# Kernel optimization log

Hardware: AMD Instinct MI355X
Metric: run time of the kernel (lower is better)

## Reference

```python
import jax, jax.numpy as jnp
import numpy as np

B, N = 4096, 512


def setup_inputs() -> dict:
    key = jax.random.key(0)
    ks = jax.random.split(key, 8)
    waypoints = jax.random.normal(ks[0], (B, N, 2), dtype=jnp.float32)
    # learned params: scalar smooth_weight + curvature_net MLP (4->64->32->1)
    smooth_weight = jnp.float32(0.3)
    W1 = jax.random.normal(ks[1], (4, 64), dtype=jnp.float32) * 0.5
    b1 = jnp.zeros((64,), dtype=jnp.float32)
    W2 = jax.random.normal(ks[2], (64, 32), dtype=jnp.float32) * 0.125
    b2 = jnp.zeros((32,), dtype=jnp.float32)
    W3 = jax.random.normal(ks[3], (32, 1), dtype=jnp.float32) * 0.18
    b3 = jnp.zeros((1,), dtype=jnp.float32)
    return {"waypoints": waypoints, "smooth_weight": smooth_weight,
            "W1": W1, "b1": b1, "W2": W2, "b2": b2, "W3": W3, "b3": b3}


def _forward(waypoints, smooth_weight, W1, b1, W2, b2, W3, b3):
    Bq, Nq, _ = waypoints.shape
    # finite differences
    d1 = waypoints[:, 1:] - waypoints[:, :-1]          # (B, N-1, 2)
    d2 = d1[:, 1:] - d1[:, :-1]                        # (B, N-2, 2)
    d1 = jnp.concatenate([d1, d1[:, -1:]], axis=1)     # (B, N, 2)
    z = jnp.zeros((Bq, 1, 2), dtype=waypoints.dtype)
    d2 = jnp.concatenate([z, d2, z], axis=1)           # (B, N, 2)
    feats = jnp.concatenate([d1, d2], axis=-1)         # (B, N, 4)
    # curvature MLP -> sigmoid weight in (0,1)
    h = jax.nn.relu(jnp.einsum('bnf,fh->bnh', feats, W1) + b1)
    h = jax.nn.relu(jnp.einsum('bnh,hk->bnk', h, W2) + b2)
    cw = jax.nn.sigmoid(jnp.einsum('bnk,ko->bno', h, W3) + b3)  # (B, N, 1)
    sw = jax.nn.sigmoid(smooth_weight)
    w = sw * (1.0 - cw[..., 0])                        # (B, N)
    # linear recurrence: y_i = w_i * y_{i-1} + (1-w_i) * x_i, y_0 = x_0
    a = jnp.swapaxes(w[:, 1:], 0, 1)                   # (N-1, B)
    x = jnp.swapaxes(waypoints[:, 1:], 0, 1)           # (N-1, B, 2)

    def step(carry, inp):
        a_i, x_i = inp
        y = a_i[:, None] * carry + (1.0 - a_i)[:, None] * x_i
        return y, y

    _, ys = jax.lax.scan(step, waypoints[:, 0], (a, x))
    smoothed = jnp.concatenate([waypoints[:, :1], jnp.swapaxes(ys, 0, 1)], axis=1)
    # endpoints pinned to original (start already equals input)
    smoothed = smoothed.at[:, -1].set(waypoints[:, -1])
    return smoothed


def reference(waypoints, smooth_weight, W1, b1, W2, b2, W3, b3):
    return _forward(waypoints, smooth_weight, W1, b1, W2, b2, W3, b3)
```

## Files before the change

kernel.cpp:

```cpp
#include <hip/hip_runtime.h>
#include <math.h>

#define NPT 512
#define BROWS 4096

typedef _Float16 half8  __attribute__((ext_vector_type(8)));
typedef _Float16 h2     __attribute__((ext_vector_type(2)));
typedef float    f32x16 __attribute__((ext_vector_type(16)));

__device__ __forceinline__ float sigmoidf_fast(float x) {
    return 1.0f / (1.0f + __expf(-x));
}

__device__ __forceinline__ h2 pkrtz(float a, float b) {
    return __builtin_bit_cast(h2, __builtin_amdgcn_cvt_pkrtz(a, b));
}

#if __has_builtin(__builtin_amdgcn_fdot2)
__device__ __forceinline__ float fdot2(h2 a, h2 b, float c) {
    return __builtin_amdgcn_fdot2(__builtin_bit_cast(__fp16 __attribute__((ext_vector_type(2))), a),
                                  __builtin_bit_cast(__fp16 __attribute__((ext_vector_type(2))), b),
                                  c, false);
}
#else
__device__ __forceinline__ float fdot2(h2 a, h2 b, float c) {
    c = fmaf((float)a[0], (float)b[0], c);
    c = fmaf((float)a[1], (float)b[1], c);
    return c;
}
#endif

union H8 { half8 v; h2 p[4]; unsigned int w[4]; };

__device__ __forceinline__ f32x16 mfma32(half8 a, half8 b, f32x16 c) {
    return __builtin_amdgcn_mfma_f32_32x32x16_f16(a, b, c, 0, 0, 0);
}

__device__ __forceinline__ void pl32swap(unsigned &a, unsigned &b) {
    asm volatile("v_permlane32_swap_b32 %0, %1" : "+v"(a), "+v"(b));
}

__device__ __forceinline__ half8 makeB2(unsigned p0, unsigned p1,
                                        unsigned p2, unsigned p3) {
    pl32swap(p0, p2);
    pl32swap(p1, p3);
    H8 B; B.w[0] = p0; B.w[1] = p1; B.w[2] = p2; B.w[3] = p3;
    return B.v;
}

__global__ __launch_bounds__(256, 4) void wps_kernel(
    const float* __restrict__ wp,
    const float* __restrict__ sww,
    const float* __restrict__ W1,
    const float* __restrict__ b1,
    const float* __restrict__ W2,
    const float* __restrict__ b2,
    const float* __restrict__ W3,
    const float* __restrict__ b3,
    float* __restrict__ out)
{
    __shared__ float sLg[2][NPT];
    __shared__ float2 sY[2];

    const int t    = threadIdx.x;
    const int lane = t & 63;
    const int wv   = t >> 6;
    const int row0 = blockIdx.x * 2;
    const int c    = lane & 31;
    const int hi   = lane >> 5;

    half8 A1t[2];
    #pragma unroll
    for (int tt = 0; tt < 2; ++tt) {
        H8 a;
        a.w[0] = 0u; a.w[1] = 0u; a.w[2] = 0u; a.w[3] = 0u;
        if (hi == 0) {
            const int ch = tt * 32 + c;
            h2 v0; v0[0] = (_Float16)W1[0 * 64 + ch]; v0[1] = (_Float16)W1[1 * 64 + ch];
            h2 v1; v1[0] = (_Float16)W1[2 * 64 + ch]; v1[1] = (_Float16)W1[3 * 64 + ch];
            h2 v2; v2[0] = (_Float16)b1[ch];          v2[1] = (_Float16)0.f;
            a.p[0] = v0; a.p[1] = v1; a.p[2] = v2;
        }
        A1t[tt] = a.v;
    }
    half8 A2s[4];
    #pragma unroll
    for (int s = 0; s < 4; ++s) {
        H8 a;
        #pragma unroll
        for (int jj = 0; jj < 4; ++jj) {
            const int k = s * 16 + hi * 8 + 2 * jj;
            h2 v; v[0] = (_Float16)W2[k * 32 + c]; v[1] = (_Float16)W2[(k + 1) * 32 + c];
            a.p[jj] = v;
        }
        A2s[s] = a.v;
    }
    h2 b2p[8], w3p[8];
    #pragma unroll
    for (int rr = 0; rr < 8; ++rr) {
        const int q   = 2 * rr;
        const int row = (q & 3) + 8 * (q >> 2) + 4 * hi;
        h2 bv; bv[0] = (_Float16)b2[row]; bv[1] = (_Float16)b2[row + 1];
        h2 wv2; wv2[0] = (_Float16)W3[row]; wv2[1] = (_Float16)W3[row + 1];
        b2p[rr] = bv;
        w3p[rr] = wv2;
    }

    h2 zeroh; zeroh[0] = (_Float16)0.f; zeroh[1] = (_Float16)0.f;
    const f32x16 zero16 = {0.f,0.f,0.f,0.f,0.f,0.f,0.f,0.f,
                           0.f,0.f,0.f,0.f,0.f,0.f,0.f,0.f};

    const int seg = wv * 128;

    #pragma unroll
    for (int r = 0; r < 2; ++r) {
        const float2* P = (const float2*)(wp + (size_t)(row0 + r) * NPT * 2);

        #pragma unroll
        for (int s2 = 0; s2 < 2; ++s2) {
            const int base = seg + s2 * 64;
            const int g    = base + lane;

            float2 p  = P[g];
            float2 pm = P[(g > 0) ? g - 1 : 0];
            float2 pp = P[(g < NPT - 1) ? g + 1 : NPT - 1];
            float d1x, d1y;
            if (g < NPT - 1) { d1x = pp.x - p.x; d1y = pp.y - p.y; }
            else             { d1x = p.x - pm.x; d1y = p.y - pm.y; }
            float d2x = 0.f, d2y = 0.f;
            if (g >= 1 && g <= NPT - 2) {
                d2x = pp.x - 2.f * p.x + pm.x;
                d2y = pp.y - 2.f * p.y + pm.y;
            }
            const int u01 = __builtin_bit_cast(int, pkrtz(d1x, d1y));
            const int u23 = __builtin_bit_cast(int, pkrtz(d2x, d2y));

            #pragma unroll
            for (int T = 0; T < 2; ++T) {
                const unsigned r01 = (unsigned)__shfl(u01, T * 32 + c);
                const unsigned r23 = (unsigned)__shfl(u23, T * 32 + c);
                H8 B1;
                B1.w[0] = r01; B1.w[1] = r23;
                B1.w[2] = 0x00003C00u; B1.w[3] = 0u;

                f32x16 pre0 = mfma32(A1t[0], B1.v, zero16);
                f32x16 pre1 = mfma32(A1t[1], B1.v, zero16);

                unsigned pw0[8], pw1[8];
                #pragma unroll
                for (int rr = 0; rr < 8; ++rr) {
                    pw0[rr] = __builtin_bit_cast(unsigned,
                        __builtin_elementwise_max(pkrtz(pre0[2*rr], pre0[2*rr+1]), zeroh));
                    pw1[rr] = __builtin_bit_cast(unsigned,
                        __builtin_elementwise_max(pkrtz(pre1[2*rr], pre1[2*rr+1]), zeroh));
                }

                f32x16 accA = zero16;
                f32x16 accB = zero16;
                accA = mfma32(A2s[0], makeB2(pw0[0], pw0[1], pw0[2], pw0[3]), accA);
                accB = mfma32(A2s[1], makeB2(pw0[4], pw0[5], pw0[6], pw0[7]), accB);
                accA = mfma32(A2s[2], makeB2(pw1[0], pw1[1], pw1[2], pw1[3]), accA);
                accB = mfma32(A2s[3], makeB2(pw1[4], pw1[5], pw1[6], pw1[7]), accB);

                float v = 0.f;
                #pragma unroll
                for (int rr = 0; rr < 8; ++rr) {
                    h2 tt2 = pkrtz(accA[2*rr] + accB[2*rr],
                                   accA[2*rr+1] + accB[2*rr+1]);
                    tt2 = tt2 + b2p[rr];
                    tt2 = __builtin_elementwise_max(tt2, zeroh);
                    v = fdot2(tt2, w3p[rr], v);
                }
                v += __shfl_xor(v, 32);
                if (lane < 32) sLg[r][base + T * 32 + lane] = v;
            }
        }
    }

    __syncthreads();

    {
        const int rloc = wv >> 1;
        const int half = wv & 1;
        const int row  = row0 + rloc;
        const float2* P = (const float2*)(wp + (size_t)row * NPT * 2);
        const float bias3 = b3[0];
        const float swv   = sigmoidf_fast(sww[0]);

        const int base = half * 256 + lane * 4;
        float wr[4];
        *reinterpret_cast<float4*>(&wr[0]) =
            *reinterpret_cast<const float4*>(&sLg[rloc][base]);

        const float4* P4 = (const float4*)P;
        float2 pts[4];
        #pragma unroll
        for (int s = 0; s < 2; ++s) {
            float4 v = P4[base / 2 + s];
            pts[2 * s].x     = v.x; pts[2 * s].y     = v.y;
            pts[2 * s + 1].x = v.z; pts[2 * s + 1].y = v.w;
        }

        float a4[4], cx4[4], cy4[4];
        float A = 1.f, Cx = 0.f, Cy = 0.f;
        #pragma unroll
        for (int i = 0; i < 4; ++i) {
            const int g = base + i;
            float a = (g == 0) ? 0.f
                               : swv * (1.f - sigmoidf_fast(wr[i] + bias3));
            float cx = (1.f - a) * pts[i].x;
            float cy = (1.f - a) * pts[i].y;
            a4[i] = a; cx4[i] = cx; cy4[i] = cy;
            Cx = fmaf(a, Cx, cx);
            Cy = fmaf(a, Cy, cy);
            A *= a;
        }
        #pragma unroll
        for (int d = 1; d < 64; d <<= 1) {
            float Ap  = __shfl_up(A, d);
            float Cpx = __shfl_up(Cx, d);
            float Cpy = __shfl_up(Cy, d);
            if (lane >= d) {
                Cx = fmaf(A, Cpx, Cx);
                Cy = fmaf(A, Cpy, Cy);
                A *= Ap;
            }
        }
        float Aex  = __shfl_up(A, 1);
        float Cxex = __shfl_up(Cx, 1);
        float Cyex = __shfl_up(Cy, 1);

        float4* orow = (float4*)(out + (size_t)row * NPT * 2);

        if (half == 0) {
            float yx = (lane == 0) ? 0.f : Cxex;
            float yy = (lane == 0) ? 0.f : Cyex;
            float ox[4], oy[4];
            #pragma unroll
            for (int i = 0; i < 4; ++i) {
                yx = fmaf(a4[i], yx, cx4[i]);
                yy = fmaf(a4[i], yy, cy4[i]);
                ox[i] = yx; oy[i] = yy;
            }
            orow[base / 2]     = make_float4(ox[0], oy[0], ox[1], oy[1]);
            orow[base / 2 + 1] = make_float4(ox[2], oy[2], ox[3], oy[3]);
            if (lane == 63) { sY[rloc].x = yx; sY[rloc].y = yy; }
        }

        __syncthreads();

        if (half == 1) {
            const float2 y255 = sY[rloc];
            float yx = (lane == 0) ? y255.x : fmaf(Aex, y255.x, Cxex);
            float yy = (lane == 0) ? y255.y : fmaf(Aex, y255.y, Cyex);
            float ox[4], oy[4];
            #pragma unroll
            for (int i = 0; i < 4; ++i) {
                yx = fmaf(a4[i], yx, cx4[i]);
                yy = fmaf(a4[i], yy, cy4[i]);
                ox[i] = yx; oy[i] = yy;
            }
            if (lane == 63) {
                float2 pe = P[NPT - 1];
                ox[3] = pe.x; oy[3] = pe.y;
            }
            orow[base / 2]     = make_float4(ox[0], oy[0], ox[1], oy[1]);
            orow[base / 2 + 1] = make_float4(ox[2], oy[2], ox[3], oy[3]);
        }
    }
}

extern "C" void kernel_launch(void* const* d_in, const int* in_sizes, int n_in,
                              void* d_out, int out_size, void* d_ws, size_t ws_size,
                              hipStream_t stream) {
    const float* wp  = (const float*)d_in[0];
    const float* sww = (const float*)d_in[1];
    const float* W1  = (const float*)d_in[2];
    const float* b1  = (const float*)d_in[3];
    const float* W2  = (const float*)d_in[4];
    const float* b2  = (const float*)d_in[5];
    const float* W3  = (const float*)d_in[6];
    const float* b3  = (const float*)d_in[7];
    float* out = (float*)d_out;

    wps_kernel<<<BROWS / 2, 256, 0, stream>>>(wp, sww, W1, b1, W2, b2, W3, b3, out);
}
```

Baseline: 27.61 us.

## Process one row per single-wave block and drop cross-wave scan handoff

Changes the work split from 256-thread blocks covering two rows to 64-thread single-wave blocks covering one row. The single wave loops over all eight 64-point segments for the MLP, then scans 8 points per lane with one wave-wide prefix scan. This removes the second block barrier and the shared-memory carry handoff between half-row waves. In exchange, each wave does four times more serial MLP work, so latency hiding relies on having more resident blocks per CU.

Result: slower. 29.31 us (+6.2%).

```diff
diff --git a/kernel.cpp b/kernel.cpp
--- a/kernel.cpp
+++ b/kernel.cpp
@@ -48,7 +48,7 @@
     return B.v;
 }
 
-__global__ __launch_bounds__(256, 4) void wps_kernel(
+__global__ __launch_bounds__(64, 4) void wps_kernel(
     const float* __restrict__ wp,
     const float* __restrict__ sww,
     const float* __restrict__ W1,
@@ -59,13 +59,10 @@
     const float* __restrict__ b3,
     float* __restrict__ out)
 {
-    __shared__ float sLg[2][NPT];
-    __shared__ float2 sY[2];
-
-    const int t    = threadIdx.x;
-    const int lane = t & 63;
-    const int wv   = t >> 6;
-    const int row0 = blockIdx.x * 2;
+    __shared__ float sLg[NPT];
+
+    const int lane = threadIdx.x & 63;
+    const int row  = blockIdx.x;
     const int c    = lane & 31;
     const int hi   = lane >> 5;
 
@@ -98,10 +95,10 @@
     h2 b2p[8], w3p[8];
     #pragma unroll
     for (int rr = 0; rr < 8; ++rr) {
-        const int q   = 2 * rr;
-        const int row = (q & 3) + 8 * (q >> 2) + 4 * hi;
-        h2 bv; bv[0] = (_Float16)b2[row]; bv[1] = (_Float16)b2[row + 1];
-        h2 wv2; wv2[0] = (_Float16)W3[row]; wv2[1] = (_Float16)W3[row + 1];
+        const int q    = 2 * rr;
+        const int drow = (q & 3) + 8 * (q >> 2) + 4 * hi;
+        h2 bv;  bv[0]  = (_Float16)b2[drow]; bv[1]  = (_Float16)b2[drow + 1];
+        h2 wv2; wv2[0] = (_Float16)W3[drow]; wv2[1] = (_Float16)W3[drow + 1];
         b2p[rr] = bv;
         w3p[rr] = wv2;
     }
@@ -110,107 +107,98 @@
     const f32x16 zero16 = {0.f,0.f,0.f,0.f,0.f,0.f,0.f,0.f,
                            0.f,0.f,0.f,0.f,0.f,0.f,0.f,0.f};
 
-    const int seg = wv * 128;
-
-    #pragma unroll
-    for (int r = 0; r < 2; ++r) {
-        const float2* P = (const float2*)(wp + (size_t)(row0 + r) * NPT * 2);
-
-        #pragma unroll
-        for (int s2 = 0; s2 < 2; ++s2) {
-            const int base = seg + s2 * 64;
-            const int g    = base + lane;
-
-            float2 p  = P[g];
-            float2 pm = P[(g > 0) ? g - 1 : 0];
-            float2 pp = P[(g < NPT - 1) ? g + 1 : NPT - 1];
-            float d1x, d1y;
-            if (g < NPT - 1) { d1x = pp.x - p.x; d1y = pp.y - p.y; }
-            else             { d1x = p.x - pm.x; d1y = p.y - pm.y; }
-            float d2x = 0.f, d2y = 0.f;
-            if (g >= 1 && g <= NPT - 2) {
-                d2x = pp.x - 2.f * p.x + pm.x;
-                d2y = pp.y - 2.f * p.y + pm.y;
+    const float2* P = (const float2*)(wp + (size_t)row * NPT * 2);
+
+    #pragma unroll 2
+    for (int s2 = 0; s2 < 8; ++s2) {
+        const int base = s2 * 64;
+        const int g    = base + lane;
+
+        float2 p  = P[g];
+        float2 pm = P[(g > 0) ? g - 1 : 0];
+        float2 pp = P[(g < NPT - 1) ? g + 1 : NPT - 1];
+        float d1x, d1y;
+        if (g < NPT - 1) { d1x = pp.x - p.x; d1y = pp.y - p.y; }
+        else             { d1x = p.x - pm.x; d1y = p.y - pm.y; }
+        float d2x = 0.f, d2y = 0.f;
+        if (g >= 1 && g <= NPT - 2) {
+            d2x = pp.x - 2.f * p.x + pm.x;
+            d2y = pp.y - 2.f * p.y + pm.y;
+        }
+        const int u01 = __builtin_bit_cast(int, pkrtz(d1x, d1y));
+        const int u23 = __builtin_bit_cast(int, pkrtz(d2x, d2y));
+
+        #pragma unroll
+        for (int T = 0; T < 2; ++T) {
+            const unsigned r01 = (unsigned)__shfl(u01, T * 32 + c);
+            const unsigned r23 = (unsigned)__shfl(u23, T * 32 + c);
+            H8 B1;
+            B1.w[0] = r01; B1.w[1] = r23;
+            B1.w[2] = 0x00003C00u; B1.w[3] = 0u;
+
+            f32x16 pre0 = mfma32(A1t[0], B1.v, zero16);
+            f32x16 pre1 = mfma32(A1t[1], B1.v, zero16);
+
+            unsigned pw0[8], pw1[8];
+            #pragma unroll
+            for (int rr = 0; rr < 8; ++rr) {
+                pw0[rr] = __builtin_bit_cast(unsigned,
+                    __builtin_elementwise_max(pkrtz(pre0[2*rr], pre0[2*rr+1]), zeroh));
+                pw1[rr] = __builtin_bit_cast(unsigned,
+                    __builtin_elementwise_max(pkrtz(pre1[2*rr], pre1[2*rr+1]), zeroh));
             }
-            const int u01 = __builtin_bit_cast(int, pkrtz(d1x, d1y));
-            const int u23 = __builtin_bit_cast(int, pkrtz(d2x, d2y));
-
+
+            f32x16 accA = zero16;
+            f32x16 accB = zero16;
+            accA = mfma32(A2s[0], makeB2(pw0[0], pw0[1], pw0[2], pw0[3]), accA);
+            accB = mfma32(A2s[1], makeB2(pw0[4], pw0[5], pw0[6], pw0[7]), accB);
+            accA = mfma32(A2s[2], makeB2(pw1[0], pw1[1], pw1[2], pw1[3]), accA);
+            accB = mfma32(A2s[3], makeB2(pw1[4], pw1[5], pw1[6], pw1[7]), accB);
+
+            float v = 0.f;
             #pragma unroll
-            for (int T = 0; T < 2; ++T) {
-                const unsigned r01 = (unsigned)__shfl(u01, T * 32 + c);
-                const unsigned r23 = (unsigned)__shfl(u23, T * 32 + c);
-                H8 B1;
-                B1.w[0] = r01; B1.w[1] = r23;
-                B1.w[2] = 0x00003C00u; B1.w[3] = 0u;
-
-                f32x16 pre0 = mfma32(A1t[0], B1.v, zero16);
-                f32x16 pre1 = mfma32(A1t[1], B1.v, zero16);
-
-                unsigned pw0[8], pw1[8];
-                #pragma unroll
-                for (int rr = 0; rr < 8; ++rr) {
-                    pw0[rr] = __builtin_bit_cast(unsigned,
-                        __builtin_elementwise_max(pkrtz(pre0[2*rr], pre0[2*rr+1]), zeroh));
-                    pw1[rr] = __builtin_bit_cast(unsigned,
-                        __builtin_elementwise_max(pkrtz(pre1[2*rr], pre1[2*rr+1]), zeroh));
-                }
-
-                f32x16 accA = zero16;
-                f32x16 accB = zero16;
-                accA = mfma32(A2s[0], makeB2(pw0[0], pw0[1], pw0[2], pw0[3]), accA);
-                accB = mfma32(A2s[1], makeB2(pw0[4], pw0[5], pw0[6], pw0[7]), accB);
-                accA = mfma32(A2s[2], makeB2(pw1[0], pw1[1], pw1[2], pw1[3]), accA);
-                accB = mfma32(A2s[3], makeB2(pw1[4], pw1[5], pw1[6], pw1[7]), accB);
-
-                float v = 0.f;
-                #pragma unroll
-                for (int rr = 0; rr < 8; ++rr) {
-                    h2 tt2 = pkrtz(accA[2*rr] + accB[2*rr],
-                                   accA[2*rr+1] + accB[2*rr+1]);
-                    tt2 = tt2 + b2p[rr];
-                    tt2 = __builtin_elementwise_max(tt2, zeroh);
-                    v = fdot2(tt2, w3p[rr], v);
-                }
-                v += __shfl_xor(v, 32);
-                if (lane < 32) sLg[r][base + T * 32 + lane] = v;
+            for (int rr = 0; rr < 8; ++rr) {
+                h2 tt2 = pkrtz(accA[2*rr] + accB[2*rr],
+                               accA[2*rr+1] + accB[2*rr+1]);
+                tt2 = tt2 + b2p[rr];
+                tt2 = __builtin_elementwise_max(tt2, zeroh);
+                v = fdot2(tt2, w3p[rr], v);
             }
+            v += __shfl_xor(v, 32);
+            if (lane < 32) sLg[base + T * 32 + lane] = v;
         }
     }
 
     __syncthreads();
 
     {
-        const int rloc = wv >> 1;
-        const int half = wv & 1;
-        const int row  = row0 + rloc;
-        const float2* P = (const float2*)(wp + (size_t)row * NPT * 2);
         const float bias3 = b3[0];
         const float swv   = sigmoidf_fast(sww[0]);
 
-        const int base = half * 256 + lane * 4;
-        float wr[4];
-        *reinterpret_cast<float4*>(&wr[0]) =
-            *reinterpret_cast<const float4*>(&sLg[rloc][base]);
+        const int base = lane * 8;
+        float wr[8];
+        *reinterpret_cast<float4*>(&wr[0]) = *reinterpret_cast<const float4*>(&sLg[base]);
+        *reinterpret_cast<float4*>(&wr[4]) = *reinterpret_cast<const float4*>(&sLg[base + 4]);
 
         const float4* P4 = (const float4*)P;
-        float2 pts[4];
-        #pragma unroll
-        for (int s = 0; s < 2; ++s) {
-            float4 v = P4[base / 2 + s];
+        float2 pts[8];
+        #pragma unroll
+        for (int s = 0; s < 4; ++s) {
+            float4 v = P4[lane * 4 + s];
             pts[2 * s].x     = v.x; pts[2 * s].y     = v.y;
             pts[2 * s + 1].x = v.z; pts[2 * s + 1].y = v.w;
         }
 
-        float a4[4], cx4[4], cy4[4];
+        float a8[8], cx8[8], cy8[8];
         float A = 1.f, Cx = 0.f, Cy = 0.f;
         #pragma unroll
-        for (int i = 0; i < 4; ++i) {
+        for (int i = 0; i < 8; ++i) {
             const int g = base + i;
             float a = (g == 0) ? 0.f
                                : swv * (1.f - sigmoidf_fast(wr[i] + bias3));
             float cx = (1.f - a) * pts[i].x;
             float cy = (1.f - a) * pts[i].y;
-            a4[i] = a; cx4[i] = cx; cy4[i] = cy;
+            a8[i] = a; cx8[i] = cx; cy8[i] = cy;
             Cx = fmaf(a, Cx, cx);
             Cy = fmaf(a, Cy, cy);
             A *= a;
@@ -226,46 +214,23 @@
                 A *= Ap;
             }
         }
-        float Aex  = __shfl_up(A, 1);
-        float Cxex = __shfl_up(Cx, 1);
-        float Cyex = __shfl_up(Cy, 1);
-
+        float yx = __shfl_up(Cx, 1);
+        float yy = __shfl_up(Cy, 1);
+        if (lane == 0) { yx = 0.f; yy = 0.f; }
+
+        float2 pe = P[NPT - 1];
         float4* orow = (float4*)(out + (size_t)row * NPT * 2);
-
-        if (half == 0) {
-            float yx = (lane == 0) ? 0.f : Cxex;
-            float yy = (lane == 0) ? 0.f : Cyex;
-            float ox[4], oy[4];
-            #pragma unroll
-            for (int i = 0; i < 4; ++i) {
-                yx = fmaf(a4[i], yx, cx4[i]);
-                yy = fmaf(a4[i], yy, cy4[i]);
-                ox[i] = yx; oy[i] = yy;
-            }
-            orow[base / 2]     = make_float4(ox[0], oy[0], ox[1], oy[1]);
-            orow[base / 2 + 1] = make_float4(ox[2], oy[2], ox[3], oy[3]);
-            if (lane == 63) { sY[rloc].x = yx; sY[rloc].y = yy; }
-        }
-
-        __syncthreads();
-
-        if (half == 1) {
-            const float2 y255 = sY[rloc];
-            float yx = (lane == 0) ? y255.x : fmaf(Aex, y255.x, Cxex);
-            float yy = (lane == 0) ? y255.y : fmaf(Aex, y255.y, Cyex);
-            float ox[4], oy[4];
-            #pragma unroll
-            for (int i = 0; i < 4; ++i) {
-                yx = fmaf(a4[i], yx, cx4[i]);
-                yy = fmaf(a4[i], yy, cy4[i]);
-                ox[i] = yx; oy[i] = yy;
-            }
-            if (lane == 63) {
-                float2 pe = P[NPT - 1];
-                ox[3] = pe.x; oy[3] = pe.y;
-            }
-            orow[base / 2]     = make_float4(ox[0], oy[0], ox[1], oy[1]);
-            orow[base / 2 + 1] = make_float4(ox[2], oy[2], ox[3], oy[3]);
+        #pragma unroll
+        for (int s2 = 0; s2 < 4; ++s2) {
+            float x0, y0v, x1, y1v;
+            { const int i = 2 * s2;
+              yx = fmaf(a8[i], yx, cx8[i]); yy = fmaf(a8[i], yy, cy8[i]);
+              x0 = yx; y0v = yy; }
+            { const int i = 2 * s2 + 1;
+              yx = fmaf(a8[i], yx, cx8[i]); yy = fmaf(a8[i], yy, cy8[i]);
+              x1 = yx; y1v = yy; }
+            if (lane == 63 && s2 == 3) { x1 = pe.x; y1v = pe.y; }
+            orow[lane * 4 + s2] = make_float4(x0, y0v, x1, y1v);
         }
     }
 }
@@ -283,5 +248,5 @@
     const float* b3  = (const float*)d_in[7];
     float* out = (float*)d_out;
 
-    wps_kernel<<<BROWS / 2, 256, 0, stream>>>(wp, sww, W1, b1, W2, b2, W3, b3, out);
-}
+    wps_kernel<<<BROWS, 64, 0, stream>>>(wp, sww, W1, b1, W2, b2, W3, b3, out);
+}
```
